# Kernel tuning notes

Measured on AMD Instinct MI355X. Metric: run time of the kernel, lower is better.

Reference implementation:

```python
import jax, jax.numpy as jnp
import numpy as np

NUM_HEADS = 8
LN_EPS = 1e-5


def setup_inputs() -> dict:
    key = jax.random.key(0)
    ks = jax.random.split(key, 12)
    B, L, D = 8, 1000, 512
    dk = D // NUM_HEADS
    max_len = 1000
    s = 1.0 / np.sqrt(D)
    return {
        "x": jax.random.normal(ks[0], (B, L, D), dtype=jnp.float32),
        "Wq": jax.random.normal(ks[1], (D, D), dtype=jnp.float32) * s,
        "bq": jnp.zeros((D,), jnp.float32),
        "Wk": jax.random.normal(ks[2], (D, D), dtype=jnp.float32) * s,
        "bk": jnp.zeros((D,), jnp.float32),
        "Wv": jax.random.normal(ks[3], (D, D), dtype=jnp.float32) * s,
        "bv": jnp.zeros((D,), jnp.float32),
        "Wo": jax.random.normal(ks[4], (D, D), dtype=jnp.float32) * s,
        "bo": jnp.zeros((D,), jnp.float32),
        "rel_pos_embed": jax.random.normal(ks[5], (2 * max_len - 1, dk), dtype=jnp.float32) * 0.05,
        "ln_gamma": jnp.ones((D,), jnp.float32),
        "ln_beta": jnp.zeros((D,), jnp.float32),
    }


def reference(x, Wq, bq, Wk, bk, Wv, bv, Wo, bo, rel_pos_embed, ln_gamma, ln_beta):
    B, L, D = x.shape
    H = NUM_HEADS
    dk = D // H
    residual = x
    # LayerNorm (pre-norm)
    mu = jnp.mean(x, axis=-1, keepdims=True)
    var = jnp.mean(jnp.square(x - mu), axis=-1, keepdims=True)
    xn = (x - mu) * jax.lax.rsqrt(var + LN_EPS) * ln_gamma + ln_beta
    # projections (torch Linear: x @ W.T + b), split heads -> (B, H, L, dk)
    q = (xn @ Wq.T + bq).reshape(B, L, H, dk).transpose(0, 2, 1, 3)
    k = (xn @ Wk.T + bk).reshape(B, L, H, dk).transpose(0, 2, 1, 3)
    v = (xn @ Wv.T + bv).reshape(B, L, H, dk).transpose(0, 2, 1, 3)
    scores = jnp.einsum("bhid,bhjd->bhij", q, k) / jnp.sqrt(jnp.float32(dk))
    # relative position bias: idx[i, j] = j - i + L - 1
    rng = jnp.arange(L)
    rel_idx = rng[None, :] - rng[:, None] + (L - 1)  # (L, L)
    rel = rel_pos_embed[rel_idx]  # (L, L, dk)
    pos_scores = jnp.einsum("bhid,ijd->bhij", q, rel)
    attn = jax.nn.softmax(scores + pos_scores, axis=-1)  # dropout = identity (eval)
    ctx = jnp.einsum("bhij,bhjd->bhid", attn, v)
    ctx = ctx.transpose(0, 2, 1, 3).reshape(B, L, D)
    out = ctx @ Wo.T + bo
    return out + residual
```

## Files before the change

### kernel.cpp

```cpp
#include <hip/hip_runtime.h>
#include <hip/hip_bf16.h>

#define NHEAD 8
#define DK 64
#define DMODEL 512
#define LSEQ 1000
#define TI 64
#define TJ 64
#define NJT 16

typedef __attribute__((ext_vector_type(8))) short bf16x8;
typedef __attribute__((ext_vector_type(4))) float f32x4;

__device__ inline short f2bf(float f) {
    __hip_bfloat16 h = __float2bfloat16(f);
    return *reinterpret_cast<short*>(&h);
}
__device__ inline float bf2f(short s) {
    unsigned int u = ((unsigned int)(unsigned short)s) << 16;
    return __uint_as_float(u);
}
__device__ inline void gload_lds16(const void* g, void* l) {
    __builtin_amdgcn_global_load_lds(
        (const __attribute__((address_space(1))) unsigned int*)g,
        (__attribute__((address_space(3))) unsigned int*)l, 16, 0, 0);
}

__global__ __launch_bounds__(256) void convert_kernel(
    const float* __restrict__ Wq, const float* __restrict__ Wk, const float* __restrict__ Wv,
    const float* __restrict__ Wo, const float* __restrict__ E,
    short* __restrict__ Wqkv_bf, short* __restrict__ Wo_bf, short* __restrict__ E_bf)
{
    int qd = blockIdx.x * 256 + threadIdx.x;
    if (qd < 196608) {
        int flat = qd * 4;
        int row = flat >> 9, col = flat & 511;
        int proj = row >> 9, rrow = row & 511;
        const float* src = proj == 0 ? Wq : (proj == 1 ? Wk : Wv);
        float sc = proj == 0 ? 0.125f : 1.0f;
        float4 x = *(const float4*)&src[(size_t)rrow * 512 + col];
        short t[4] = { f2bf(x.x * sc), f2bf(x.y * sc), f2bf(x.z * sc), f2bf(x.w * sc) };
        *(uint2*)&Wqkv_bf[flat] = *(uint2*)t;
    } else if (qd < 262144) {
        int flat = (qd - 196608) * 4;
        float4 x = *(const float4*)&Wo[flat];
        short t[4] = { f2bf(x.x), f2bf(x.y), f2bf(x.z), f2bf(x.w) };
        *(uint2*)&Wo_bf[flat] = *(uint2*)t;
    } else if (qd < 294128) {
        int flat = (qd - 262144) * 4;
        float4 x = *(const float4*)&E[flat];
        short t[4] = { f2bf(x.x * 8.f), f2bf(x.y * 8.f), f2bf(x.z * 8.f), f2bf(x.w * 8.f) };
        *(uint2*)&E_bf[flat] = *(uint2*)t;
    }
}

__global__ __launch_bounds__(256) void ln_kernel(
    const float* __restrict__ x, const float* __restrict__ gamma,
    const float* __restrict__ beta, short* __restrict__ xn)
{
    int row = blockIdx.x;
    int tid = threadIdx.x;
    const float2* xr = (const float2*)(x + (size_t)row * DMODEL);
    float2 v = xr[tid];
    float s  = v.x + v.y;
    float ss = v.x * v.x + v.y * v.y;
#pragma unroll
    for (int o = 32; o > 0; o >>= 1) {
        s  += __shfl_down(s, o, 64);
        ss += __shfl_down(ss, o, 64);
    }
    __shared__ float red[8];
    int wid = tid >> 6;
    if ((tid & 63) == 0) { red[wid * 2] = s; red[wid * 2 + 1] = ss; }
    __syncthreads();
    s  = red[0] + red[2] + red[4] + red[6];
    ss = red[1] + red[3] + red[5] + red[7];
    float mu  = s * (1.0f / (float)DMODEL);
    float var = ss * (1.0f / (float)DMODEL) - mu * mu;
    float inv = rsqrtf(var + 1e-5f);
    float2 g  = ((const float2*)gamma)[tid];
    float2 bb = ((const float2*)beta)[tid];
    short o2[2];
    o2[0] = f2bf((v.x - mu) * inv * g.x + bb.x);
    o2[1] = f2bf((v.y - mu) * inv * g.y + bb.y);
    *(unsigned int*)&xn[(size_t)row * DMODEL + tid * 2] = *(unsigned int*)o2;
}

template<int MODE>
__global__ __launch_bounds__(256) void gemm_bf16(
    const short* __restrict__ A, const short* __restrict__ W,
    const float* __restrict__ b0, const float* __restrict__ b1, const float* __restrict__ b2,
    short* __restrict__ Oq, short* __restrict__ Ok, short* __restrict__ Ov,
    float* __restrict__ Of, const float* __restrict__ resid)
{
    __shared__ short As[128 * 32];
    __shared__ short Bs[128 * 32];
    const int K = 512;
    const int tid = threadIdx.x;
    const int lane = tid & 63, w = tid >> 6;
    const int m0 = blockIdx.y * 128, n0 = blockIdx.x * 128;
    const int wr = w >> 1, wc = w & 1;

    const int srow = (lane >> 2);
    const int scol = (lane & 3) * 8;
    int ga0 = m0 + (w * 2 + 0) * 16 + srow; if (ga0 > 7999) ga0 = 7999;
    int ga1 = m0 + (w * 2 + 1) * 16 + srow; if (ga1 > 7999) ga1 = 7999;
    const int gb0 = n0 + (w * 2 + 0) * 16 + srow;
    const int gb1 = n0 + (w * 2 + 1) * 16 + srow;

    f32x4 acc[4][4];
#pragma unroll
    for (int i = 0; i < 4; ++i)
#pragma unroll
        for (int j = 0; j < 4; ++j) acc[i][j] = (f32x4){0.f, 0.f, 0.f, 0.f};

    for (int k0 = 0; k0 < K; k0 += 32) {
        __syncthreads();
        gload_lds16(&A[(size_t)ga0 * K + k0 + scol], &As[(w * 2 + 0) * 512]);
        gload_lds16(&A[(size_t)ga1 * K + k0 + scol], &As[(w * 2 + 1) * 512]);
        gload_lds16(&W[(size_t)gb0 * K + k0 + scol], &Bs[(w * 2 + 0) * 512]);
        gload_lds16(&W[(size_t)gb1 * K + k0 + scol], &Bs[(w * 2 + 1) * 512]);
        __syncthreads();

        bf16x8 af[4], bf[4];
#pragma unroll
        for (int fi = 0; fi < 4; ++fi)
            af[fi] = *(bf16x8*)&As[(wr * 64 + fi * 16 + (lane & 15)) * 32 + (lane >> 4) * 8];
#pragma unroll
        for (int fj = 0; fj < 4; ++fj)
            bf[fj] = *(bf16x8*)&Bs[(wc * 64 + fj * 16 + (lane & 15)) * 32 + (lane >> 4) * 8];
#pragma unroll
        for (int fi = 0; fi < 4; ++fi)
#pragma unroll
            for (int fj = 0; fj < 4; ++fj)
                acc[fi][fj] = __builtin_amdgcn_mfma_f32_16x16x32_bf16(af[fi], bf[fj], acc[fi][fj], 0, 0, 0);
    }

#pragma unroll
    for (int fi = 0; fi < 4; ++fi) {
#pragma unroll
        for (int fj = 0; fj < 4; ++fj) {
#pragma unroll
            for (int r = 0; r < 4; ++r) {
                int m = m0 + wr * 64 + fi * 16 + (lane >> 4) * 4 + r;
                if (m >= 8000) continue;
                int n = n0 + wc * 64 + fj * 16 + (lane & 15);
                float val = acc[fi][fj][r];
                if (MODE == 0) {
                    int proj = n >> 9, rem = n & 511;
                    int h = rem >> 6, d = rem & 63;
                    float bias = proj == 0 ? b0[rem] * 0.125f : (proj == 1 ? b1[rem] : b2[rem]);
                    short* O = proj == 0 ? Oq : (proj == 1 ? Ok : Ov);
                    int bb = m / 1000, ii = m - bb * 1000;
                    O[((size_t)(bb * NHEAD + h) * LSEQ + ii) * DK + d] = f2bf(val + bias);
                } else {
                    Of[(size_t)m * DMODEL + n] = val + b0[n] + resid[(size_t)m * DMODEL + n];
                }
            }
        }
    }
}

__global__ __launch_bounds__(256, 4) void attn_mfma(
    const short* __restrict__ q, const short* __restrict__ k,
    const short* __restrict__ v, const short* __restrict__ E,
    short* __restrict__ ctx)
{
    __shared__ short QsPl[TI][72];
    __shared__ short Kt[TJ][72];
    __shared__ short Vt[DK][72];
    __shared__ short Pp[TI][92];

    const int it = blockIdx.x, h = blockIdx.y, b = blockIdx.z;
    const int i0 = it * TI;
    const int tid = threadIdx.x;
    const int lane = tid & 63, w = tid >> 6;
    const int g = lane >> 4, c = lane & 15;

    const size_t base = (size_t)(b * NHEAD + h) * LSEQ * DK;

#pragma unroll
    for (int rep = 0; rep < 2; ++rep) {
        int id = tid + rep * 256;
        int row = id >> 3, c0 = (id & 7) * 8;
        int gr = i0 + row; if (gr > LSEQ - 1) gr = LSEQ - 1;
        *(int4*)&QsPl[row][c0] = *(const int4*)&q[base + (size_t)gr * DK + c0];
    }
    __syncthreads();

    bf16x8 Aq0 = *(bf16x8*)&QsPl[w * 16 + c][g * 8];
    bf16x8 Aq1 = *(bf16x8*)&QsPl[w * 16 + c][32 + g * 8];

    float mrow[4], lrow[4];
    f32x4 acc[4];
#pragma unroll
    for (int r = 0; r < 4; ++r) { mrow[r] = -1e30f; lrow[r] = 0.f; }
#pragma unroll
    for (int fd = 0; fd < 4; ++fd) acc[fd] = (f32x4){0.f, 0.f, 0.f, 0.f};

    for (int jt = 0; jt < NJT; ++jt) {
        const int j0 = jt * TJ;
        const int d0 = j0 - i0 + (LSEQ - 1) - 63;
        __syncthreads();

#pragma unroll
        for (int rep = 0; rep < 2; ++rep) {
            int id = tid + rep * 256;
            int row = id >> 3, c0 = (id & 7) * 8;
            int gr = j0 + row; if (gr > LSEQ - 1) gr = LSEQ - 1;
            *(int4*)&Kt[row][c0] = *(const int4*)&k[base + (size_t)gr * DK + c0];
        }
#pragma unroll
        for (int rep = 0; rep < 4; ++rep) {
            int id = tid + rep * 256;
            int j = ((id >> 8) << 4) | (id & 15);
            int dq = ((id >> 4) & 15) * 4;
            int gr = j0 + j; if (gr > LSEQ - 1) gr = LSEQ - 1;
            short t[4];
            *(int2*)t = *(const int2*)&v[base + (size_t)gr * DK + dq];
            Vt[dq + 0][j] = t[0];
            Vt[dq + 1][j] = t[1];
            Vt[dq + 2][j] = t[2];
            Vt[dq + 3][j] = t[3];
        }
        bf16x8 ef[5][2];
#pragma unroll
        for (int fdl = 0; fdl < 5; ++fdl) {
            int dd = d0 + (3 - w + fdl) * 16 + c;
            if (dd < 0) dd = 0;
            if (dd > 2 * LSEQ - 2) dd = 2 * LSEQ - 2;
            const short* erow = E + (size_t)dd * DK;
            ef[fdl][0] = *(const bf16x8*)&erow[g * 8];
            ef[fdl][1] = *(const bf16x8*)&erow[32 + g * 8];
        }
        __syncthreads();

#pragma unroll
        for (int fdl = 0; fdl < 5; ++fdl) {
            f32x4 pa = (f32x4){0.f, 0.f, 0.f, 0.f};
            pa = __builtin_amdgcn_mfma_f32_16x16x32_bf16(Aq0, ef[fdl][0], pa, 0, 0, 0);
            pa = __builtin_amdgcn_mfma_f32_16x16x32_bf16(Aq1, ef[fdl][1], pa, 0, 0, 0);
#pragma unroll
            for (int r = 0; r < 4; ++r)
                Pp[w * 16 + g * 4 + r][fdl * 16 + c] = f2bf(pa[r]);
        }

        f32x4 sf[4];
#pragma unroll
        for (int fj = 0; fj < 4; ++fj) {
            f32x4 s4 = (f32x4){0.f, 0.f, 0.f, 0.f};
            bf16x8 k0v = *(bf16x8*)&Kt[fj * 16 + c][g * 8];
            bf16x8 k1v = *(bf16x8*)&Kt[fj * 16 + c][32 + g * 8];
            s4 = __builtin_amdgcn_mfma_f32_16x16x32_bf16(Aq0, k0v, s4, 0, 0, 0);
            s4 = __builtin_amdgcn_mfma_f32_16x16x32_bf16(Aq1, k1v, s4, 0, 0, 0);
            sf[fj] = s4;
        }

        float sv[4][4], pm[4];
#pragma unroll
        for (int r = 0; r < 4; ++r) pm[r] = -1e30f;
#pragma unroll
        for (int fj = 0; fj < 4; ++fj) {
            int jl = fj * 16 + c;
            bool valid = (j0 + jl) < LSEQ;
#pragma unroll
            for (int r = 0; r < 4; ++r) {
                int ilt = w * 16 + g * 4 + r;
                int dl = fj * 16 + 15 + c - (g * 4 + r);
                float x = sf[fj][r] + bf2f(Pp[ilt][dl]);
                if (!valid) x = -1e30f;
                sv[fj][r] = x;
                pm[r] = fmaxf(pm[r], x);
            }
        }
#pragma unroll
        for (int r = 0; r < 4; ++r) {
            float vv = pm[r];
            vv = fmaxf(vv, __shfl_xor(vv, 1));
            vv = fmaxf(vv, __shfl_xor(vv, 2));
            vv = fmaxf(vv, __shfl_xor(vv, 4));
            vv = fmaxf(vv, __shfl_xor(vv, 8));
            pm[r] = vv;
        }
        float psum[4];
#pragma unroll
        for (int r = 0; r < 4; ++r) {
            float mn = fmaxf(mrow[r], pm[r]);
            float sc = __expf(mrow[r] - mn);
            mrow[r] = mn;
            lrow[r] *= sc;
#pragma unroll
            for (int fd = 0; fd < 4; ++fd) acc[fd][r] *= sc;
            psum[r] = 0.f;
        }
#pragma unroll
        for (int fj = 0; fj < 4; ++fj) {
            int jl = fj * 16 + c;
#pragma unroll
            for (int r = 0; r < 4; ++r) {
                float p = __expf(sv[fj][r] - mrow[r]);
                psum[r] += p;
                QsPl[w * 16 + g * 4 + r][jl] = f2bf(p);
            }
        }
#pragma unroll
        for (int r = 0; r < 4; ++r) {
            float vv = psum[r];
            vv += __shfl_xor(vv, 1);
            vv += __shfl_xor(vv, 2);
            vv += __shfl_xor(vv, 4);
            vv += __shfl_xor(vv, 8);
            lrow[r] += vv;
        }

#pragma unroll
        for (int ks = 0; ks < 2; ++ks) {
            bf16x8 ap = *(bf16x8*)&QsPl[w * 16 + c][ks * 32 + g * 8];
#pragma unroll
            for (int fd = 0; fd < 4; ++fd) {
                bf16x8 bv2 = *(bf16x8*)&Vt[fd * 16 + c][ks * 32 + g * 8];
                acc[fd] = __builtin_amdgcn_mfma_f32_16x16x32_bf16(ap, bv2, acc[fd], 0, 0, 0);
            }
        }
    }

#pragma unroll
    for (int r = 0; r < 4; ++r) {
        int ig = i0 + w * 16 + g * 4 + r;
        if (ig < LSEQ) {
            float inv = 1.0f / lrow[r];
#pragma unroll
            for (int fd = 0; fd < 4; ++fd)
                ctx[((size_t)(b * LSEQ + ig)) * DMODEL + h * DK + fd * 16 + c] =
                    f2bf(acc[fd][r] * inv);
        }
    }
}

extern "C" void kernel_launch(void* const* d_in, const int* in_sizes, int n_in,
                              void* d_out, int out_size, void* d_ws, size_t ws_size,
                              hipStream_t stream)
{
    const float* x     = (const float*)d_in[0];
    const float* Wq    = (const float*)d_in[1];
    const float* bq    = (const float*)d_in[2];
    const float* Wk    = (const float*)d_in[3];
    const float* bk    = (const float*)d_in[4];
    const float* Wv    = (const float*)d_in[5];
    const float* bv    = (const float*)d_in[6];
    const float* Wo    = (const float*)d_in[7];
    const float* bo    = (const float*)d_in[8];
    const float* E     = (const float*)d_in[9];
    const float* gamma = (const float*)d_in[10];
    const float* beta  = (const float*)d_in[11];
    float* out = (float*)d_out;

    const size_t nTok = 8 * LSEQ;
    const size_t nBLD = nTok * DMODEL;
    short* xn_bf   = (short*)d_ws;
    short* qb      = xn_bf + nBLD;
    short* kb      = qb + nBLD;
    short* vb      = kb + nBLD;
    short* ctx_bf  = vb + nBLD;
    short* Wqkv_bf = ctx_bf + nBLD;
    short* Wo_bf   = Wqkv_bf + 1536 * 512;
    short* E_bf    = Wo_bf + 512 * 512;

    convert_kernel<<<1149, 256, 0, stream>>>(Wq, Wk, Wv, Wo, E, Wqkv_bf, Wo_bf, E_bf);
    ln_kernel<<<(int)nTok, 256, 0, stream>>>(x, gamma, beta, xn_bf);
    gemm_bf16<0><<<dim3(12, 63), 256, 0, stream>>>(
        xn_bf, Wqkv_bf, bq, bk, bv, qb, kb, vb, nullptr, nullptr);
    attn_mfma<<<dim3((LSEQ + TI - 1) / TI, NHEAD, 8), 256, 0, stream>>>(
        qb, kb, vb, E_bf, ctx_bf);
    gemm_bf16<1><<<dim3(4, 63), 256, 0, stream>>>(
        ctx_bf, Wo_bf, bo, nullptr, nullptr, nullptr, nullptr, nullptr, out, x);
}
```

Measured before the change: 269.1 us.

## Prefetch next K, V and relative-embedding tiles into registers during compute

Global loads of the next K, V and positional-embedding tiles are issued into registers right after the positional MFMA step, so their latency overlaps the QK, softmax and PV work of the current tile. At the start of the next iteration the registers are simply stored to LDS. This raises register pressure (kreg, vreg and ef stay live across the loop), which could lower occupancy under launch_bounds(256,4). The score buffer sv is folded into sf to save registers.

```diff
diff --git a/kernel.cpp b/kernel.cpp
--- a/kernel.cpp
+++ b/kernel.cpp
@@ -179,6 +179,46 @@
 
     const size_t base = (size_t)(b * NHEAD + h) * LSEQ * DK;
 
+    const int krow0 = tid >> 3;
+    const int kc0   = (tid & 7) * 8;
+    int4 kreg[2];
+    int2 vreg[4];
+    bf16x8 ef[5][2];
+
+    auto load_k = [&](int jt_) {
+#pragma unroll
+        for (int rep = 0; rep < 2; ++rep) {
+            int gr = jt_ * TJ + krow0 + rep * 32;
+            if (gr > LSEQ - 1) gr = LSEQ - 1;
+            kreg[rep] = *(const int4*)&k[base + (size_t)gr * DK + kc0];
+        }
+    };
+    auto load_v = [&](int jt_) {
+#pragma unroll
+        for (int rep = 0; rep < 4; ++rep) {
+            int id = tid + rep * 256;
+            int j = ((id >> 8) << 4) | (id & 15);
+            int dq = ((id >> 4) & 15) * 4;
+            int gr = jt_ * TJ + j;
+            if (gr > LSEQ - 1) gr = LSEQ - 1;
+            vreg[rep] = *(const int2*)&v[base + (size_t)gr * DK + dq];
+        }
+    };
+    auto load_e = [&](int jt_) {
+        int d0_ = jt_ * TJ - i0 + (LSEQ - 1) - 63;
+#pragma unroll
+        for (int fdl = 0; fdl < 5; ++fdl) {
+            int dd = d0_ + (3 - w + fdl) * 16 + c;
+            if (dd < 0) dd = 0;
+            if (dd > 2 * LSEQ - 2) dd = 2 * LSEQ - 2;
+            const short* erow = E + (size_t)dd * DK;
+            ef[fdl][0] = *(const bf16x8*)&erow[g * 8];
+            ef[fdl][1] = *(const bf16x8*)&erow[32 + g * 8];
+        }
+    };
+
+    load_k(0); load_v(0); load_e(0);
+
 #pragma unroll
     for (int rep = 0; rep < 2; ++rep) {
         int id = tid + rep * 256;
@@ -200,39 +240,23 @@
 
     for (int jt = 0; jt < NJT; ++jt) {
         const int j0 = jt * TJ;
-        const int d0 = j0 - i0 + (LSEQ - 1) - 63;
         __syncthreads();
 
 #pragma unroll
-        for (int rep = 0; rep < 2; ++rep) {
-            int id = tid + rep * 256;
-            int row = id >> 3, c0 = (id & 7) * 8;
-            int gr = j0 + row; if (gr > LSEQ - 1) gr = LSEQ - 1;
-            *(int4*)&Kt[row][c0] = *(const int4*)&k[base + (size_t)gr * DK + c0];
-        }
+        for (int rep = 0; rep < 2; ++rep)
+            *(int4*)&Kt[krow0 + rep * 32][kc0] = kreg[rep];
 #pragma unroll
         for (int rep = 0; rep < 4; ++rep) {
             int id = tid + rep * 256;
             int j = ((id >> 8) << 4) | (id & 15);
             int dq = ((id >> 4) & 15) * 4;
-            int gr = j0 + j; if (gr > LSEQ - 1) gr = LSEQ - 1;
             short t[4];
-            *(int2*)t = *(const int2*)&v[base + (size_t)gr * DK + dq];
+            *(int2*)t = vreg[rep];
             Vt[dq + 0][j] = t[0];
             Vt[dq + 1][j] = t[1];
             Vt[dq + 2][j] = t[2];
             Vt[dq + 3][j] = t[3];
         }
-        bf16x8 ef[5][2];
-#pragma unroll
-        for (int fdl = 0; fdl < 5; ++fdl) {
-            int dd = d0 + (3 - w + fdl) * 16 + c;
-            if (dd < 0) dd = 0;
-            if (dd > 2 * LSEQ - 2) dd = 2 * LSEQ - 2;
-            const short* erow = E + (size_t)dd * DK;
-            ef[fdl][0] = *(const bf16x8*)&erow[g * 8];
-            ef[fdl][1] = *(const bf16x8*)&erow[32 + g * 8];
-        }
         __syncthreads();
 
 #pragma unroll
@@ -244,6 +268,8 @@
             for (int r = 0; r < 4; ++r)
                 Pp[w * 16 + g * 4 + r][fdl * 16 + c] = f2bf(pa[r]);
         }
+
+        if (jt + 1 < NJT) { load_k(jt + 1); load_v(jt + 1); load_e(jt + 1); }
 
         f32x4 sf[4];
 #pragma unroll
@@ -256,7 +282,7 @@
             sf[fj] = s4;
         }
 
-        float sv[4][4], pm[4];
+        float pm[4];
 #pragma unroll
         for (int r = 0; r < 4; ++r) pm[r] = -1e30f;
 #pragma unroll
@@ -269,7 +295,7 @@
                 int dl = fj * 16 + 15 + c - (g * 4 + r);
                 float x = sf[fj][r] + bf2f(Pp[ilt][dl]);
                 if (!valid) x = -1e30f;
-                sv[fj][r] = x;
+                sf[fj][r] = x;
                 pm[r] = fmaxf(pm[r], x);
             }
         }
@@ -298,7 +324,7 @@
             int jl = fj * 16 + c;
 #pragma unroll
             for (int r = 0; r < 4; ++r) {
-                float p = __expf(sv[fj][r] - mrow[r]);
+                float p = __expf(sf[fj][r] - mrow[r]);
                 psum[r] += p;
                 QsPl[w * 16 + g * 4 + r][jl] = f2bf(p);
             }
```

New measurement: 293.6 us. 1.09x slower.

## Prefetch next K/V and positional-embedding tiles into registers during compute

Applied to the files above, without the earlier changes.

The attention loop now issues global loads for the next tile's K, V and relative-position embedding fragments into registers right after the positional MFMAs. They are written to shared memory at the start of the next iteration, so memory latency overlaps with the QK, softmax and PV work instead of stalling each tile. This holds extra registers live across the loop body (about 28 VGPRs for prefetch), which could pressure occupancy under the 256x4 launch bound. The score array is also reused in place to save registers.

```diff
diff --git a/kernel.cpp b/kernel.cpp
--- a/kernel.cpp
+++ b/kernel.cpp
@@ -161,6 +161,49 @@
     }
 }
 
+#define CLAMPROW(r) ((r) > LSEQ - 1 ? LSEQ - 1 : (r))
+#define CLAMPE(r)   ((r) < 0 ? 0 : ((r) > 2 * LSEQ - 2 ? 2 * LSEQ - 2 : (r)))
+
+#define LOAD_KV(JT) do {                                                          \
+    int gr_;                                                                      \
+    gr_ = CLAMPROW((JT) * TJ + krow0);      kreg0 = *(const int4*)&k[base + (size_t)gr_ * DK + kc0]; \
+    gr_ = CLAMPROW((JT) * TJ + krow0 + 32); kreg1 = *(const int4*)&k[base + (size_t)gr_ * DK + kc0]; \
+    gr_ = CLAMPROW((JT) * TJ + vj);         vreg0 = *(const int2*)&v[base + (size_t)gr_ * DK + vdq]; \
+    gr_ = CLAMPROW((JT) * TJ + 16 + vj);    vreg1 = *(const int2*)&v[base + (size_t)gr_ * DK + vdq]; \
+    gr_ = CLAMPROW((JT) * TJ + 32 + vj);    vreg2 = *(const int2*)&v[base + (size_t)gr_ * DK + vdq]; \
+    gr_ = CLAMPROW((JT) * TJ + 48 + vj);    vreg3 = *(const int2*)&v[base + (size_t)gr_ * DK + vdq]; \
+} while (0)
+
+#define LOAD_E1(JT, FDL, EA, EB) do {                                             \
+    int dd_ = CLAMPE((JT) * TJ - i0 + (LSEQ - 1) - 63 + (3 - w + (FDL)) * 16 + c);\
+    const short* er_ = E + (size_t)dd_ * DK;                                      \
+    EA = *(const bf16x8*)&er_[g * 8];                                             \
+    EB = *(const bf16x8*)&er_[32 + g * 8];                                        \
+} while (0)
+
+#define LOAD_E(JT) do {                                                           \
+    LOAD_E1(JT, 0, ef00, ef01); LOAD_E1(JT, 1, ef10, ef11);                       \
+    LOAD_E1(JT, 2, ef20, ef21); LOAD_E1(JT, 3, ef30, ef31);                       \
+    LOAD_E1(JT, 4, ef40, ef41);                                                   \
+} while (0)
+
+#define POS_MFMA(FDL, EA, EB) do {                                                \
+    f32x4 pa_ = (f32x4){0.f, 0.f, 0.f, 0.f};                                      \
+    pa_ = __builtin_amdgcn_mfma_f32_16x16x32_bf16(Aq0, EA, pa_, 0, 0, 0);         \
+    pa_ = __builtin_amdgcn_mfma_f32_16x16x32_bf16(Aq1, EB, pa_, 0, 0, 0);         \
+    Pp[w * 16 + g * 4 + 0][(FDL) * 16 + c] = f2bf(pa_[0]);                        \
+    Pp[w * 16 + g * 4 + 1][(FDL) * 16 + c] = f2bf(pa_[1]);                        \
+    Pp[w * 16 + g * 4 + 2][(FDL) * 16 + c] = f2bf(pa_[2]);                        \
+    Pp[w * 16 + g * 4 + 3][(FDL) * 16 + c] = f2bf(pa_[3]);                        \
+} while (0)
+
+#define STORE_V(VR, JOFF) do {                                                    \
+    Vt[vdq + 0][(JOFF) + vj] = (short)((unsigned)(VR).x & 0xFFFF);                \
+    Vt[vdq + 1][(JOFF) + vj] = (short)((unsigned)(VR).x >> 16);                   \
+    Vt[vdq + 2][(JOFF) + vj] = (short)((unsigned)(VR).y & 0xFFFF);                \
+    Vt[vdq + 3][(JOFF) + vj] = (short)((unsigned)(VR).y >> 16);                   \
+} while (0)
+
 __global__ __launch_bounds__(256, 4) void attn_mfma(
     const short* __restrict__ q, const short* __restrict__ k,
     const short* __restrict__ v, const short* __restrict__ E,
@@ -179,6 +222,18 @@
 
     const size_t base = (size_t)(b * NHEAD + h) * LSEQ * DK;
 
+    const int krow0 = tid >> 3;
+    const int kc0   = (tid & 7) * 8;
+    const int vj    = tid & 15;
+    const int vdq   = (tid >> 4) * 4;
+
+    int4 kreg0, kreg1;
+    int2 vreg0, vreg1, vreg2, vreg3;
+    bf16x8 ef00, ef01, ef10, ef11, ef20, ef21, ef30, ef31, ef40, ef41;
+
+    LOAD_KV(0);
+    LOAD_E(0);
+
 #pragma unroll
     for (int rep = 0; rep < 2; ++rep) {
         int id = tid + rep * 256;
@@ -200,49 +255,25 @@
 
     for (int jt = 0; jt < NJT; ++jt) {
         const int j0 = jt * TJ;
-        const int d0 = j0 - i0 + (LSEQ - 1) - 63;
         __syncthreads();
 
-#pragma unroll
-        for (int rep = 0; rep < 2; ++rep) {
-            int id = tid + rep * 256;
-            int row = id >> 3, c0 = (id & 7) * 8;
-            int gr = j0 + row; if (gr > LSEQ - 1) gr = LSEQ - 1;
-            *(int4*)&Kt[row][c0] = *(const int4*)&k[base + (size_t)gr * DK + c0];
-        }
-#pragma unroll
-        for (int rep = 0; rep < 4; ++rep) {
-            int id = tid + rep * 256;
-            int j = ((id >> 8) << 4) | (id & 15);
-            int dq = ((id >> 4) & 15) * 4;
-            int gr = j0 + j; if (gr > LSEQ - 1) gr = LSEQ - 1;
-            short t[4];
-            *(int2*)t = *(const int2*)&v[base + (size_t)gr * DK + dq];
-            Vt[dq + 0][j] = t[0];
-            Vt[dq + 1][j] = t[1];
-            Vt[dq + 2][j] = t[2];
-            Vt[dq + 3][j] = t[3];
-        }
-        bf16x8 ef[5][2];
-#pragma unroll
-        for (int fdl = 0; fdl < 5; ++fdl) {
-            int dd = d0 + (3 - w + fdl) * 16 + c;
-            if (dd < 0) dd = 0;
-            if (dd > 2 * LSEQ - 2) dd = 2 * LSEQ - 2;
-            const short* erow = E + (size_t)dd * DK;
-            ef[fdl][0] = *(const bf16x8*)&erow[g * 8];
-            ef[fdl][1] = *(const bf16x8*)&erow[32 + g * 8];
-        }
+        *(int4*)&Kt[krow0][kc0] = kreg0;
+        *(int4*)&Kt[krow0 + 32][kc0] = kreg1;
+        STORE_V(vreg0, 0);
+        STORE_V(vreg1, 16);
+        STORE_V(vreg2, 32);
+        STORE_V(vreg3, 48);
         __syncthreads();
 
-#pragma unroll
-        for (int fdl = 0; fdl < 5; ++fdl) {
-            f32x4 pa = (f32x4){0.f, 0.f, 0.f, 0.f};
-            pa = __builtin_amdgcn_mfma_f32_16x16x32_bf16(Aq0, ef[fdl][0], pa, 0, 0, 0);
-            pa = __builtin_amdgcn_mfma_f32_16x16x32_bf16(Aq1, ef[fdl][1], pa, 0, 0, 0);
-#pragma unroll
-            for (int r = 0; r < 4; ++r)
-                Pp[w * 16 + g * 4 + r][fdl * 16 + c] = f2bf(pa[r]);
+        POS_MFMA(0, ef00, ef01);
+        POS_MFMA(1, ef10, ef11);
+        POS_MFMA(2, ef20, ef21);
+        POS_MFMA(3, ef30, ef31);
+        POS_MFMA(4, ef40, ef41);
+
+        if (jt + 1 < NJT) {
+            LOAD_KV(jt + 1);
+            LOAD_E(jt + 1);
         }
 
         f32x4 sf[4];
@@ -256,7 +287,7 @@
             sf[fj] = s4;
         }
 
-        float sv[4][4], pm[4];
+        float pm[4];
 #pragma unroll
         for (int r = 0; r < 4; ++r) pm[r] = -1e30f;
 #pragma unroll
@@ -269,7 +300,7 @@
                 int dl = fj * 16 + 15 + c - (g * 4 + r);
                 float x = sf[fj][r] + bf2f(Pp[ilt][dl]);
                 if (!valid) x = -1e30f;
-                sv[fj][r] = x;
+                sf[fj][r] = x;
                 pm[r] = fmaxf(pm[r], x);
             }
         }
@@ -298,7 +329,7 @@
             int jl = fj * 16 + c;
 #pragma unroll
             for (int r = 0; r < 4; ++r) {
-                float p = __expf(sv[fj][r] - mrow[r]);
+                float p = __expf(sf[fj][r] - mrow[r]);
                 psum[r] += p;
                 QsPl[w * 16 + g * 4 + r][jl] = f2bf(p);
             }
```

After: 412.9 us. +53.4%, slower.
